# Optimization experiments

Hardware: AMD Instinct MI355X
Metric: run time of the kernel (lower is better)

Reference implementation:

```python
import jax, jax.numpy as jnp
import numpy as np

B, N, C = 4, 48 * 64, 256
H, W = 48, 64


def _positional_encodings(batch, dtype=jnp.float32):
    # (x^2, y^2, xy, x, y, 1) encoding; matches get_positional_encodings with intrinsics=None
    ys = jnp.linspace(-1.0, 1.0, H, dtype=dtype)
    xs = jnp.linspace(-1.0, 1.0, W, dtype=dtype)
    p3 = jnp.tile(ys, W)            # [N] : ys repeated W times (torch .repeat(B, w))
    p4 = jnp.repeat(xs, H)          # [N] : each x repeated H times (repeat_interleave)
    pos = jnp.stack([p3 * p3, p4 * p4, p3 * p4, p3, p4, jnp.ones_like(p3)], axis=-1)  # [N,6]
    return jnp.broadcast_to(pos, (batch, N, 6))


def setup_inputs() -> dict:
    key = jax.random.key(0)
    k1, k2, k3, k4 = jax.random.split(key, 4)
    x1 = jax.random.normal(k1, (B, N, C), dtype=jnp.float32)
    x2 = jax.random.normal(k2, (B, N, C), dtype=jnp.float32)
    corr = jax.random.normal(k3, (B, 1, H, W, H, W), dtype=jnp.float32)
    W_proj = jax.random.normal(k4, (C + 6, C), dtype=jnp.float32) * (1.0 / np.sqrt(C + 6))
    b_proj = jnp.zeros((C,), dtype=jnp.float32)
    return {"x1": x1, "x2": x2, "corr": corr, "W_proj": W_proj, "b_proj": b_proj}


def reference(x1, x2, corr, W_proj, b_proj):
    b, n, c = x1.shape
    a = corr.reshape(b, n, n)                      # squeeze(1) + double flatten
    # dual softmax (row-wise * column-wise)
    s_row = jax.nn.softmax(a, axis=-1)
    s_col = jax.nn.softmax(a, axis=-2)
    attn_f1 = s_row * s_col                        # [B,N,N]
    attn_f2 = jnp.swapaxes(attn_f1, -2, -1)        # softmax(a^T,-1)*softmax(a^T,-2) == attn_f1^T

    pos = _positional_encodings(b, dtype=x1.dtype)
    v1 = jnp.concatenate([x1, pos], axis=2)        # [B,N,C+6]
    v2 = jnp.concatenate([x2, pos], axis=2)

    # bilinear products v^T @ attn @ v  -> [B, C+6, C+6]
    fund1 = jnp.einsum('bnc,bnm,bmd->bcd', v1, attn_f1, v1)
    fund2 = jnp.einsum('bnc,bnm,bmd->bcd', v2, attn_f2, v2)

    fund1 = jnp.swapaxes(fund1, -2, -1)
    fund2 = jnp.swapaxes(fund2, -2, -1)

    out1 = fund1 @ W_proj + b_proj                 # proj_fundamental
    out2 = fund2 @ W_proj + b_proj
    return (out2, out1)                            # (fundamental_2, fundamental_1)
```

## Files before the change

kernel.cpp:

```cpp
#include <hip/hip_runtime.h>
#include <math.h>

#define NB 4
#define NN 3072
#define NC 256
#define CP 262
#define KG 384
#define XW 528
#define MD 272
#define K3S 4
#define HH 48
#define WW 64
#define LOG2E 1.4426950408889634f

typedef short short8 __attribute__((ext_vector_type(8)));
typedef short short4v __attribute__((ext_vector_type(4)));
typedef float f32x4 __attribute__((ext_vector_type(4)));
typedef unsigned int uint4v __attribute__((ext_vector_type(4)));

__device__ __forceinline__ float fexp2(float x) {
#if __has_builtin(__builtin_amdgcn_exp2f)
    return __builtin_amdgcn_exp2f(x);
#else
    return __exp2f(x);
#endif
}

__device__ __forceinline__ void bsplit(float v, short& h, short& l) {
    unsigned u = __float_as_uint(v);
    h = (short)(u >> 16);
    float r = v - __uint_as_float(u & 0xFFFF0000u);
    l = (short)(__float_as_uint(r) >> 16);
}

__device__ __forceinline__ void fma4(float4& c, float a, float4 b) {
    c.x = fmaf(a, b.x, c.x);
    c.y = fmaf(a, b.y, c.y);
    c.z = fmaf(a, b.z, c.z);
    c.w = fmaf(a, b.w, c.w);
}

__global__ __launch_bounds__(256) void k_stats(const float* __restrict__ corr,
                                               const float* __restrict__ x1,
                                               const float* __restrict__ x2,
                                               float* __restrict__ pSum,
                                               float* __restrict__ rlS,
                                               short* __restrict__ Xh, short* __restrict__ Xl) {
    int bid = blockIdx.x;
    int t = threadIdx.x;
    if (bid < 384) {
        int cx = bid % 12;
        int b = (bid / 12) & 3;
        int ch = bid / 48;
        int m = cx * 256 + t;
        const float* p = corr + (size_t)b * NN * NN + (size_t)ch * 384 * NN + m;
        float s0 = 0.f, s1 = 0.f, s2 = 0.f, s3 = 0.f;
        for (int r = 0; r < 384; r += 4) {
            s0 += __expf(p[(size_t)(r + 0) * NN]);
            s1 += __expf(p[(size_t)(r + 1) * NN]);
            s2 += __expf(p[(size_t)(r + 2) * NN]);
            s3 += __expf(p[(size_t)(r + 3) * NN]);
        }
        pSum[((size_t)ch * NB + b) * NN + m] = (s0 + s1) + (s2 + s3);
    } else if (bid < 3456) {
        int rid = bid - 384;
        int b = rid / 768;
        int r0 = (rid - b * 768) * 4;
        int w = t >> 6, l = t & 63;
        int n = r0 + w;
        const float4* p = (const float4*)(corr + ((size_t)b * NN + n) * NN);
        float s = 0.f;
#pragma unroll
        for (int i = 0; i < 12; i++) {
            float4 v = p[l + i * 64];
            s += __expf(v.x) + __expf(v.y) + __expf(v.z) + __expf(v.w);
        }
#pragma unroll
        for (int off = 1; off < 64; off <<= 1) s += __shfl_xor(s, off);
        if (l == 0) rlS[b * NN + n] = __log2f(s);
    } else {
        int id = (bid - 3456) * 256 + t;
        int col = id % XW;
        int rest = id / XW;
        int kg = rest % KG;
        int b = rest / KG;
        short* ph = Xh + (size_t)id * 8;
        short* pl = Xl + (size_t)id * 8;
        if (col < 512) {
            const float* src = (col < 256 ? x1 : x2) + ((size_t)b * NN + kg * 8) * NC + (col & 255);
#pragma unroll
            for (int j = 0; j < 8; j++) {
                short hs, ls;
                bsplit(src[(size_t)j * NC], hs, ls);
                ph[j] = hs; pl[j] = ls;
            }
        } else {
            int c = col - 512;
#pragma unroll
            for (int j = 0; j < 8; j++) {
                int k = kg * 8 + j;
                int ip4 = k / HH;
                int ip3 = k - ip4 * HH;
                float p3 = -1.f + 2.f * (float)ip3 / 47.f;
                float p4 = -1.f + 2.f * (float)ip4 / 63.f;
                float v = 0.f;
                if (c == 0) v = p3 * p3;
                else if (c == 1) v = p4 * p4;
                else if (c == 2) v = p3 * p4;
                else if (c == 3) v = p3;
                else if (c == 4) v = p4;
                else if (c == 5) v = 1.f;
                short hs, ls;
                bsplit(v, hs, ls);
                ph[j] = hs; pl[j] = ls;
            }
        }
    }
}

__global__ __launch_bounds__(256) void k_comb(const float* __restrict__ pSum,
                                              float* __restrict__ ccS) {
    int idx = blockIdx.x * 256 + threadIdx.x;
    float s = 0.f;
#pragma unroll
    for (int ch = 0; ch < 8; ch++) s += pSum[(size_t)ch * NB * NN + idx];
    ccS[idx] = __log2f(s);
}

struct SMemMain {
    unsigned AH[2][48 * 32];
    unsigned AL[2][48 * 32];
    float ccsh[NN];
};
union SMemU {
    SMemMain m;
    float pdump[2 * 64 * 12];
};

#define LOAD_B4(PH, PL, BHF, BLF)                                            \
    {                                                                        \
        _Pragma("unroll") for (int i_ = 0; i_ < 4; i_++) {                   \
            BHF[i_] = *(const short8*)((PH) + i_ * 128);                     \
            BLF[i_] = *(const short8*)((PL) + i_ * 128);                     \
        }                                                                    \
    }

#define READ_AFRAGS3(BUFH, BUFL, UNIT, AHF, ALF)                             \
    {                                                                        \
        _Pragma("unroll") for (int fr_ = 0; fr_ < 3; fr_++) {                \
            int rowr_ = fr_ * 16 + row16;                                    \
            int uidx_ = rowr_ * 32 + (((UNIT) ^ (rowr_ & 7)) << 2);          \
            AHF[fr_] = *(const short8*)&(BUFH)[uidx_];                       \
            ALF[fr_] = *(const short8*)&(BUFL)[uidx_];                       \
        }                                                                    \
    }

#define MFMA_CLUSTER34(AHF, ALF, BHF, BLF)                                                         \
    {                                                                                              \
        _Pragma("unroll") for (int fr_ = 0; fr_ < 3; fr_++)                                        \
        _Pragma("unroll") for (int i_ = 0; i_ < 4; i_++)                                           \
            acc[fr_][i_] = __builtin_amdgcn_mfma_f32_16x16x32_bf16(AHF[fr_], BHF[i_], acc[fr_][i_], 0, 0, 0); \
        _Pragma("unroll") for (int fr_ = 0; fr_ < 3; fr_++)                                        \
        _Pragma("unroll") for (int i_ = 0; i_ < 4; i_++)                                           \
            acc[fr_][i_] = __builtin_amdgcn_mfma_f32_16x16x32_bf16(AHF[fr_], BLF[i_], acc[fr_][i_], 0, 0, 0); \
        _Pragma("unroll") for (int fr_ = 0; fr_ < 3; fr_++)                                        \
        _Pragma("unroll") for (int i_ = 0; i_ < 4; i_++)                                           \
            acc[fr_][i_] = __builtin_amdgcn_mfma_f32_16x16x32_bf16(ALF[fr_], BHF[i_], acc[fr_][i_], 0, 0, 0); \
    }

#define POS_CLUSTER3(AHF, ALF, PBH, PBL)                                                           \
    {                                                                                              \
        _Pragma("unroll") for (int fr_ = 0; fr_ < 3; fr_++) {                                      \
            accP[fr_] = __builtin_amdgcn_mfma_f32_16x16x32_bf16(AHF[fr_], (PBH), accP[fr_], 0, 0, 0); \
            accP[fr_] = __builtin_amdgcn_mfma_f32_16x16x32_bf16(AHF[fr_], (PBL), accP[fr_], 0, 0, 0); \
            accP[fr_] = __builtin_amdgcn_mfma_f32_16x16x32_bf16(ALF[fr_], (PBH), accP[fr_], 0, 0, 0); \
        }                                                                                          \
    }

#define STAGE_A8(DSTH, DSTL, PC)                                                                  \
    {                                                                                             \
        f32x4 ccv0 = *(const f32x4*)&ccsh[(PC) * 64 + g * 8];                                     \
        f32x4 ccv1 = *(const f32x4*)&ccsh[(PC) * 64 + g * 8 + 4];                                 \
        float ev[8];                                                                              \
        _Pragma("unroll") for (int q_ = 0; q_ < 4; q_++) {                                        \
            ev[q_]     = fexp2(fmaf(C2, cr0[q_], rmn) - ccv0[q_]);                                \
            ev[4 + q_] = fexp2(fmaf(C2, cr1[q_], rmn) - ccv1[q_]);                                \
        }                                                                                         \
        uint4v hi, lo;                                                                            \
        _Pragma("unroll") for (int q_ = 0; q_ < 4; q_++) {                                        \
            unsigned u0 = __float_as_uint(ev[2 * q_]);                                            \
            unsigned u1 = __float_as_uint(ev[2 * q_ + 1]);                                        \
            hi[q_] = __builtin_amdgcn_perm(u1, u0, 0x07060302u);                                  \
            float r0_ = ev[2 * q_] - __uint_as_float(u0 & 0xffff0000u);                           \
            float r1_ = ev[2 * q_ + 1] - __uint_as_float(u1 & 0xffff0000u);                       \
            lo[q_] = __builtin_amdgcn_perm(__float_as_uint(r1_), __float_as_uint(r0_), 0x07060302u); \
        }                                                                                         \
        *(uint4v*)&(DSTH)[widx] = hi;                                                             \
        *(uint4v*)&(DSTL)[widx] = lo;                                                             \
    }

__global__ __launch_bounds__(512, 2) void k2_mfma(const float* __restrict__ corr,
        const short* __restrict__ Xh, const short* __restrict__ Xl,
        const float* __restrict__ rlS, const float* __restrict__ ccS,
        short* __restrict__ Zh, short* __restrict__ Zl) {
    __shared__ SMemU sm;
    float* ccsh = sm.m.ccsh;

    const float C2 = 2.f * LOG2E;
    const size_t BSTEP = (size_t)4 * XW * 8;

    int bid = blockIdx.x;
    int xcd = bid & 7, sub = bid >> 3;
    int b = xcd >> 1;
    int rowblk = (xcd & 1) + (sub << 1);
    int n0 = rowblk * 48;

    int t = threadIdx.x;
    int w = t >> 6, l = t & 63;
    int row16 = l & 15, slot = l >> 4;
    bool duty6 = (w == 6);
    bool duty7 = (w == 7);
    bool writer = (t < 384);
    int wrow = t >> 3, g = t & 7;
    int widx = wrow * 32 + ((g ^ (wrow & 7)) << 2);

    {
        const f32x4* src = (const f32x4*)(ccS + (size_t)b * NN);
        for (int i = t; i < NN / 4; i += 512) ((f32x4*)ccsh)[i] = src[i];
    }

    const float* corrR = corr;
    float rmn = 0.f;
    if (writer) {
        corrR = corr + ((size_t)b * NN + n0 + wrow) * NN + g * 8;
        rmn = -rlS[b * NN + n0 + wrow];
    }

    int col0 = w * 64 + row16;
    const short* bh = Xh + ((size_t)(b * KG + slot) * XW + col0) * 8;
    const short* bl = Xl + ((size_t)(b * KG + slot) * XW + col0) * 8;

    f32x4 acc[3][4];
    f32x4 accP[3];
    const f32x4 zz = {0.f, 0.f, 0.f, 0.f};
#pragma unroll
    for (int fr = 0; fr < 3; fr++) {
#pragma unroll
        for (int i = 0; i < 4; i++) acc[fr][i] = zz;
        accP[fr] = zz;
    }

    short8 BhA[4], BlA[4], BhB[4], BlB[4];
    short8 P0h = {0,0,0,0,0,0,0,0}, P0l = P0h, P1h = P0h, P1l = P0h;
    LOAD_B4(bh, bl, BhA, BlA);

    f32x4 cr0, cr1;
    __syncthreads();
    if (writer) {
        cr0 = *(const f32x4*)(corrR);
        cr1 = *(const f32x4*)(corrR + 4);
        STAGE_A8(sm.m.AH[0], sm.m.AL[0], 0);
        cr0 = *(const f32x4*)(corrR + 64);
        cr1 = *(const f32x4*)(corrR + 68);
    }
    asm volatile("s_waitcnt lgkmcnt(0)" ::: "memory");
    __builtin_amdgcn_s_barrier();

    int cur = 0;
    for (int p = 0; p < 48; ++p) {
        const unsigned* AHc = &sm.m.AH[cur][0];
        const unsigned* ALc = &sm.m.AL[cur][0];
        unsigned* AHn = &sm.m.AH[cur ^ 1][0];
        unsigned* ALn = &sm.m.AL[cur ^ 1][0];
        short8 Ah[3], Al[3];
        READ_AFRAGS3(AHc, ALc, slot, Ah, Al);
        bh += BSTEP; bl += BSTEP;
        LOAD_B4(bh, bl, BhB, BlB);
        if (duty6) {
            size_t o0 = ((size_t)(b * KG + p * 8 + slot) * XW + 512 + row16) * 8;
            P0h = *(const short8*)(Xh + o0);
            P0l = *(const short8*)(Xl + o0);
        }
        MFMA_CLUSTER34(Ah, Al, BhA, BlA);
        if (duty6) POS_CLUSTER3(Ah, Al, P0h, P0l);
        READ_AFRAGS3(AHc, ALc, 4 + slot, Ah, Al);
        if (p < 47) {
            bh += BSTEP; bl += BSTEP;
            LOAD_B4(bh, bl, BhA, BlA);
        }
        if (duty7) {
            size_t o1 = ((size_t)(b * KG + p * 8 + 4 + slot) * XW + 512 + row16) * 8;
            P1h = *(const short8*)(Xh + o1);
            P1l = *(const short8*)(Xl + o1);
        }
        if (writer) {
            int pc = (p + 1 < 48) ? p + 1 : 47;
            STAGE_A8(AHn, ALn, pc);
            int pn = (p + 2 < 48) ? p + 2 : 47;
            cr0 = *(const f32x4*)(corrR + pn * 64);
            cr1 = *(const f32x4*)(corrR + pn * 64 + 4);
        }
        MFMA_CLUSTER34(Ah, Al, BhB, BlB);
        if (duty7) POS_CLUSTER3(Ah, Al, P1h, P1l);
        asm volatile("s_waitcnt lgkmcnt(0)" ::: "memory");
        __builtin_amdgcn_s_barrier();
        cur ^= 1;
    }

#pragma unroll
    for (int fr = 0; fr < 3; fr++) {
        int kgz = rowblk * 6 + fr * 2 + (slot >> 1);
        int jb = (slot & 1) << 2;
#pragma unroll
        for (int i = 0; i < 4; i++) {
            int colv = w * 64 + i * 16 + row16;
            size_t off = ((size_t)(b * KG + kgz) * XW + colv) * 8 + jb;
            short4v zh, zl;
#pragma unroll
            for (int r = 0; r < 4; r++) {
                short hs, ls; bsplit(acc[fr][i][r], hs, ls);
                zh[r] = hs; zl[r] = ls;
            }
            *(short4v*)(Zh + off) = zh;
            *(short4v*)(Zl + off) = zl;
        }
    }
    if (w >= 6) {
#pragma unroll
        for (int fr = 0; fr < 3; fr++)
            *(f32x4*)&sm.pdump[(size_t)((w - 6) * 64 + l) * 12 + fr * 4] = accP[fr];
    }
    __syncthreads();
    if (t < 192) {
        int fr = t >> 6, ll = t & 63;
        int sl = ll >> 4, r16 = ll & 15;
        f32x4 s = *(const f32x4*)&sm.pdump[(size_t)ll * 12 + fr * 4]
                + *(const f32x4*)&sm.pdump[(size_t)(64 + ll) * 12 + fr * 4];
        int kgz = rowblk * 6 + fr * 2 + (sl >> 1);
        int jb = (sl & 1) << 2;
        size_t off = ((size_t)(b * KG + kgz) * XW + 512 + r16) * 8 + jb;
        short4v zh, zl;
#pragma unroll
        for (int r = 0; r < 4; r++) {
            short hs, ls; bsplit(s[r], hs, ls);
            zh[r] = hs; zl[r] = ls;
        }
        *(short4v*)(Zh + off) = zh;
        *(short4v*)(Zl + off) = zl;
    }
}

__global__ __launch_bounds__(256) void k3_mfma(const short* __restrict__ Xh, const short* __restrict__ Xl,
                                               const short* __restrict__ Zh, const short* __restrict__ Zl,
                                               float* __restrict__ Mpart) {
    int tile = blockIdx.x;
    int rt = tile / 3, ct = tile % 3;
    int mb = blockIdx.y;
    int mat = mb >> 2, b = mb & 3;
    int split = blockIdx.z;

    const int O0[4] = {0, 6, 12, 17};
    int r0f = O0[rt], rNf = O0[rt + 1] - r0f;
    int c0f = O0[ct], cNf = O0[ct + 1] - c0f;

    int t = threadIdx.x;
    int w = t >> 6, l = t & 63;
    int row16 = l & 15, slot = l >> 4;
    int wr = w >> 1, wc = w & 1;
    int rh = (rNf + 1) >> 1;
    int rbeg = r0f + (wr ? rh : 0);
    int rcnt = wr ? (rNf - rh) : rh;
    int chh = (cNf + 1) >> 1;
    int cbeg = c0f + (wc ? chh : 0);
    int ccnt = wc ? (cNf - chh) : chh;

    const short *Ah_, *Al_, *Bh_, *Bl_;
    int abase, bbase;
    if (mat == 0) { Ah_ = Xh; Al_ = Xl; Bh_ = Zh; Bl_ = Zl; abase = 0; bbase = 0; }
    else          { Ah_ = Zh; Al_ = Zl; Bh_ = Xh; Bl_ = Xl; abase = 256; bbase = 256; }

    int acol[3], bcol[3];
#pragma unroll
    for (int i = 0; i < 3; i++) {
        int fa = rbeg + i;
        acol[i] = ((fa < 16) ? (abase + fa * 16) : 512) + row16;
        int fb = cbeg + i;
        bcol[i] = ((fb < 16) ? (bbase + fb * 16) : 512) + row16;
    }

    f32x4 acc[3][3];
    const f32x4 zz = {0.f, 0.f, 0.f, 0.f};
#pragma unroll
    for (int i = 0; i < 3; i++)
#pragma unroll
        for (int j = 0; j < 3; j++) acc[i][j] = zz;

    for (int it = 0; it < 24; it++) {
        int kg = split * 96 + it * 4 + slot;
        size_t base = (size_t)(b * KG + kg) * XW;
        short8 Ah[3], Al[3], Bhf[3], Blf[3];
#pragma unroll
        for (int i = 0; i < 3; i++) {
            if (i < rcnt) {
                Ah[i] = *(const short8*)(Ah_ + (base + acol[i]) * 8);
                Al[i] = *(const short8*)(Al_ + (base + acol[i]) * 8);
            }
            if (i < ccnt) {
                Bhf[i] = *(const short8*)(Bh_ + (base + bcol[i]) * 8);
                Blf[i] = *(const short8*)(Bl_ + (base + bcol[i]) * 8);
            }
        }
#pragma unroll
        for (int i = 0; i < 3; i++) {
            if (i < rcnt) {
#pragma unroll
                for (int j = 0; j < 3; j++) {
                    if (j < ccnt) {
                        acc[i][j] = __builtin_amdgcn_mfma_f32_16x16x32_bf16(Ah[i], Bhf[j], acc[i][j], 0, 0, 0);
                        acc[i][j] = __builtin_amdgcn_mfma_f32_16x16x32_bf16(Al[i], Bhf[j], acc[i][j], 0, 0, 0);
                        acc[i][j] = __builtin_amdgcn_mfma_f32_16x16x32_bf16(Ah[i], Blf[j], acc[i][j], 0, 0, 0);
                    }
                }
            }
        }
    }

    float* Mp = Mpart + (size_t)(mb * K3S + split) * (MD * MD);
#pragma unroll
    for (int i = 0; i < 3; i++) {
        if (i < rcnt) {
#pragma unroll
            for (int j = 0; j < 3; j++) {
                if (j < ccnt) {
                    int r = (rbeg + i) * 16 + slot * 4;
                    int c = (cbeg + j) * 16 + row16;
#pragma unroll
                    for (int q = 0; q < 4; q++)
                        Mp[(size_t)(r + q) * MD + c] = acc[i][j][q];
                }
            }
        }
    }
}

__global__ __launch_bounds__(256) void k_mcombine(const float* __restrict__ Mpart, float* __restrict__ M) {
    const int per = MD * MD;
    int f4 = blockIdx.x * 256 + threadIdx.x;
    if (f4 >= (8 * per) / 4) return;
    int e = f4 * 4;
    int mb = e / per;
    int off = e - mb * per;
    const float* src = Mpart + (size_t)mb * K3S * per + off;
    float4 s = make_float4(0.f, 0.f, 0.f, 0.f);
#pragma unroll
    for (int sp = 0; sp < K3S; sp++) {
        float4 v = *(const float4*)(src + (size_t)sp * per);
        s.x += v.x; s.y += v.y; s.z += v.z; s.w += v.w;
    }
    *(float4*)(M + (size_t)mb * per + off) = s;
}

__global__ __launch_bounds__(256) void k4_proj(const float* __restrict__ M, const float* __restrict__ Wp,
                                               const float* __restrict__ bp, float* __restrict__ out) {
    int i0 = blockIdx.x * 16;
    int b = blockIdx.y;
    int mat = blockIdx.z;
    const float* Mp = M + (size_t)(mat * 4 + b) * (MD * MD);
    int t = threadIdx.x;
    int jt = t & 63, it = t >> 6;
    int j = jt * 4;
    float4 a0 = make_float4(0.f, 0.f, 0.f, 0.f), a1 = a0, a2 = a0, a3 = a0;
#pragma unroll 2
    for (int k = 0; k < CP; k++) {
        float4 w = *(const float4*)(Wp + (size_t)k * NC + j);
        float4 g = *(const float4*)(Mp + (size_t)k * MD + i0 + it * 4);
        fma4(a0, g.x, w); fma4(a1, g.y, w); fma4(a2, g.z, w); fma4(a3, g.w, w);
    }
    float4 bb = *(const float4*)(bp + j);
    a0.x += bb.x; a0.y += bb.y; a0.z += bb.z; a0.w += bb.w;
    a1.x += bb.x; a1.y += bb.y; a1.z += bb.z; a1.w += bb.w;
    a2.x += bb.x; a2.y += bb.y; a2.z += bb.z; a2.w += bb.w;
    a3.x += bb.x; a3.y += bb.y; a3.z += bb.z; a3.w += bb.w;
    float* ob = out + (mat == 0 ? (size_t)NB * CP * NC : (size_t)0) + (size_t)b * CP * NC;
    int i = i0 + it * 4;
    if (i + 0 < CP) *(float4*)(ob + (size_t)(i + 0) * NC + j) = a0;
    if (i + 1 < CP) *(float4*)(ob + (size_t)(i + 1) * NC + j) = a1;
    if (i + 2 < CP) *(float4*)(ob + (size_t)(i + 2) * NC + j) = a2;
    if (i + 3 < CP) *(float4*)(ob + (size_t)(i + 3) * NC + j) = a3;
}

extern "C" void kernel_launch(void* const* d_in, const int* in_sizes, int n_in,
                              void* d_out, int out_size, void* d_ws, size_t ws_size,
                              hipStream_t stream) {
    const float* x1 = (const float*)d_in[0];
    const float* x2 = (const float*)d_in[1];
    const float* corr = (const float*)d_in[2];
    const float* Wp = (const float*)d_in[3];
    const float* bp = (const float*)d_in[4];
    float* out = (float*)d_out;
    float* w = (float*)d_ws;

    const size_t XSZ = (size_t)NB * KG * XW * 8;

    size_t o = 0;
    float* rlS = w + o;   o += NB * NN;
    float* ccS = w + o;   o += NB * NN;
    float* pSum = w + o;  o += 8 * NB * NN;
    short* Xh = (short*)(w + o); o += XSZ / 2;
    short* Xl = (short*)(w + o); o += XSZ / 2;
    short* Zh = (short*)(w + o); o += XSZ / 2;
    short* Zl = (short*)(w + o); o += XSZ / 2;
    float* Mpart = w + o; o += (size_t)8 * K3S * MD * MD;
    float* M = w + o;     o += (size_t)8 * MD * MD;

    k_stats<<<dim3(6624), dim3(256), 0, stream>>>(corr, x1, x2, pSum, rlS, Xh, Xl);
    k_comb<<<dim3(48), dim3(256), 0, stream>>>(pSum, ccS);
    k2_mfma<<<dim3(256), dim3(512), 0, stream>>>(corr, Xh, Xl, rlS, ccS, Zh, Zl);
    k3_mfma<<<dim3(9, 8, K3S), dim3(256), 0, stream>>>(Xh, Xl, Zh, Zl, Mpart);
    k_mcombine<<<dim3(578), dim3(256), 0, stream>>>(Mpart, M);
    k4_proj<<<dim3(17, NB, 2), dim3(256), 0, stream>>>(M, Wp, bp, out);
}
```

Before: 256.4 us.

## Fuse softmax statistics and X split into main kernel with grid barriers

```diff
diff --git a/kernel.cpp b/kernel.cpp
--- a/kernel.cpp
+++ b/kernel.cpp
@@ -38,93 +38,6 @@
     c.y = fmaf(a, b.y, c.y);
     c.z = fmaf(a, b.z, c.z);
     c.w = fmaf(a, b.w, c.w);
-}
-
-__global__ __launch_bounds__(256) void k_stats(const float* __restrict__ corr,
-                                               const float* __restrict__ x1,
-                                               const float* __restrict__ x2,
-                                               float* __restrict__ pSum,
-                                               float* __restrict__ rlS,
-                                               short* __restrict__ Xh, short* __restrict__ Xl) {
-    int bid = blockIdx.x;
-    int t = threadIdx.x;
-    if (bid < 384) {
-        int cx = bid % 12;
-        int b = (bid / 12) & 3;
-        int ch = bid / 48;
-        int m = cx * 256 + t;
-        const float* p = corr + (size_t)b * NN * NN + (size_t)ch * 384 * NN + m;
-        float s0 = 0.f, s1 = 0.f, s2 = 0.f, s3 = 0.f;
-        for (int r = 0; r < 384; r += 4) {
-            s0 += __expf(p[(size_t)(r + 0) * NN]);
-            s1 += __expf(p[(size_t)(r + 1) * NN]);
-            s2 += __expf(p[(size_t)(r + 2) * NN]);
-            s3 += __expf(p[(size_t)(r + 3) * NN]);
-        }
-        pSum[((size_t)ch * NB + b) * NN + m] = (s0 + s1) + (s2 + s3);
-    } else if (bid < 3456) {
-        int rid = bid - 384;
-        int b = rid / 768;
-        int r0 = (rid - b * 768) * 4;
-        int w = t >> 6, l = t & 63;
-        int n = r0 + w;
-        const float4* p = (const float4*)(corr + ((size_t)b * NN + n) * NN);
-        float s = 0.f;
-#pragma unroll
-        for (int i = 0; i < 12; i++) {
-            float4 v = p[l + i * 64];
-            s += __expf(v.x) + __expf(v.y) + __expf(v.z) + __expf(v.w);
-        }
-#pragma unroll
-        for (int off = 1; off < 64; off <<= 1) s += __shfl_xor(s, off);
-        if (l == 0) rlS[b * NN + n] = __log2f(s);
-    } else {
-        int id = (bid - 3456) * 256 + t;
-        int col = id % XW;
-        int rest = id / XW;
-        int kg = rest % KG;
-        int b = rest / KG;
-        short* ph = Xh + (size_t)id * 8;
-        short* pl = Xl + (size_t)id * 8;
-        if (col < 512) {
-            const float* src = (col < 256 ? x1 : x2) + ((size_t)b * NN + kg * 8) * NC + (col & 255);
-#pragma unroll
-            for (int j = 0; j < 8; j++) {
-                short hs, ls;
-                bsplit(src[(size_t)j * NC], hs, ls);
-                ph[j] = hs; pl[j] = ls;
-            }
-        } else {
-            int c = col - 512;
-#pragma unroll
-            for (int j = 0; j < 8; j++) {
-                int k = kg * 8 + j;
-                int ip4 = k / HH;
-                int ip3 = k - ip4 * HH;
-                float p3 = -1.f + 2.f * (float)ip3 / 47.f;
-                float p4 = -1.f + 2.f * (float)ip4 / 63.f;
-                float v = 0.f;
-                if (c == 0) v = p3 * p3;
-                else if (c == 1) v = p4 * p4;
-                else if (c == 2) v = p3 * p4;
-                else if (c == 3) v = p3;
-                else if (c == 4) v = p4;
-                else if (c == 5) v = 1.f;
-                short hs, ls;
-                bsplit(v, hs, ls);
-                ph[j] = hs; pl[j] = ls;
-            }
-        }
-    }
-}
-
-__global__ __launch_bounds__(256) void k_comb(const float* __restrict__ pSum,
-                                              float* __restrict__ ccS) {
-    int idx = blockIdx.x * 256 + threadIdx.x;
-    float s = 0.f;
-#pragma unroll
-    for (int ch = 0; ch < 8; ch++) s += pSum[(size_t)ch * NB * NN + idx];
-    ccS[idx] = __log2f(s);
 }
 
 struct SMemMain {
@@ -199,11 +112,14 @@
         *(uint4v*)&(DSTL)[widx] = lo;                                                             \
     }
 
-__global__ __launch_bounds__(512, 2) void k2_mfma(const float* __restrict__ corr,
-        const short* __restrict__ Xh, const short* __restrict__ Xl,
-        const float* __restrict__ rlS, const float* __restrict__ ccS,
-        short* __restrict__ Zh, short* __restrict__ Zl) {
+__global__ __launch_bounds__(512, 2) void k2_fused(const float* __restrict__ corr,
+        const float* __restrict__ x1, const float* __restrict__ x2,
+        short* __restrict__ Xh, short* __restrict__ Xl,
+        short* __restrict__ Zh, short* __restrict__ Zl,
+        float* __restrict__ colpart, float* __restrict__ ccS,
+        int* __restrict__ ctr1, int* __restrict__ ctr2) {
     __shared__ SMemU sm;
+    __shared__ float rls_sh[48];
     float* ccsh = sm.m.ccsh;
 
     const float C2 = 2.f * LOG2E;
@@ -218,23 +134,122 @@
     int t = threadIdx.x;
     int w = t >> 6, l = t & 63;
     int row16 = l & 15, slot = l >> 4;
+    const f32x4 zz = {0.f, 0.f, 0.f, 0.f};
+
+    for (int i = t; i < NN; i += 512) ccsh[i] = 0.f;
+    __syncthreads();
+
+    f32x4 cpa[12];
+#pragma unroll
+    for (int i = 0; i < 12; i++) cpa[i] = zz;
+    for (int rr = 0; rr < 6; rr++) {
+        const f32x4* rp = (const f32x4*)(corr + ((size_t)b * NN + n0 + w * 6 + rr) * NN);
+        float rsum = 0.f;
+#pragma unroll
+        for (int i = 0; i < 12; i++) {
+            f32x4 v = rp[l + i * 64];
+            f32x4 e;
+            e[0] = __expf(v[0]); e[1] = __expf(v[1]);
+            e[2] = __expf(v[2]); e[3] = __expf(v[3]);
+            cpa[i] += e;
+            rsum += (e[0] + e[1]) + (e[2] + e[3]);
+        }
+#pragma unroll
+        for (int off = 1; off < 64; off <<= 1) rsum += __shfl_xor(rsum, off);
+        if (l == 0) rls_sh[w * 6 + rr] = __log2f(rsum);
+    }
+    for (int wv = 0; wv < 8; wv++) {
+        if (w == wv) {
+#pragma unroll
+            for (int i = 0; i < 12; i++) {
+                f32x4* dst = (f32x4*)&ccsh[4 * (l + 64 * i)];
+                *dst += cpa[i];
+            }
+        }
+        __syncthreads();
+    }
+
+    for (int it = t; it < 3168; it += 512) {
+        int col = it % 528;
+        int kgl = it / 528;
+        int kg = rowblk * 6 + kgl;
+        short* ph = Xh + ((size_t)(b * KG + kg) * XW + col) * 8;
+        short* pl = Xl + ((size_t)(b * KG + kg) * XW + col) * 8;
+        if (col < 512) {
+            const float* src = (col < 256 ? x1 : x2) + ((size_t)b * NN + kg * 8) * NC + (col & 255);
+#pragma unroll
+            for (int j = 0; j < 8; j++) {
+                short hs, ls;
+                bsplit(src[(size_t)j * NC], hs, ls);
+                ph[j] = hs; pl[j] = ls;
+            }
+        } else {
+            int c = col - 512;
+#pragma unroll
+            for (int j = 0; j < 8; j++) {
+                int k = kg * 8 + j;
+                int ip4 = k / HH;
+                int ip3 = k - ip4 * HH;
+                float p3 = -1.f + 2.f * (float)ip3 / 47.f;
+                float p4 = -1.f + 2.f * (float)ip4 / 63.f;
+                float v = 0.f;
+                if (c == 0) v = p3 * p3;
+                else if (c == 1) v = p4 * p4;
+                else if (c == 2) v = p3 * p4;
+                else if (c == 3) v = p3;
+                else if (c == 4) v = p4;
+                else if (c == 5) v = 1.f;
+                short hs, ls;
+                bsplit(v, hs, ls);
+                ph[j] = hs; pl[j] = ls;
+            }
+        }
+    }
+
+    {
+        float* cp = colpart + (size_t)(b * 64 + rowblk) * NN;
+        for (int i = t; i < NN; i += 512) cp[i] = ccsh[i];
+    }
+    __syncthreads();
+    if (t == 0) {
+        __threadfence();
+        atomicAdd(ctr1 + b, 1);
+        while (__hip_atomic_load(ctr1 + b, __ATOMIC_ACQUIRE, __HIP_MEMORY_SCOPE_AGENT) < 64)
+            __builtin_amdgcn_s_sleep(8);
+    }
+    __syncthreads();
+
+    if (t < 48) {
+        const float* cp = colpart + (size_t)(b * 64) * NN + rowblk * 48 + t;
+        float s0 = 0.f, s1 = 0.f, s2 = 0.f, s3 = 0.f;
+        for (int s = 0; s < 64; s += 4) {
+            s0 += cp[(size_t)(s + 0) * NN];
+            s1 += cp[(size_t)(s + 1) * NN];
+            s2 += cp[(size_t)(s + 2) * NN];
+            s3 += cp[(size_t)(s + 3) * NN];
+        }
+        ccS[(size_t)b * NN + rowblk * 48 + t] = __log2f((s0 + s1) + (s2 + s3));
+    }
+    __syncthreads();
+    if (t == 0) {
+        __threadfence();
+        atomicAdd(ctr2 + b, 1);
+        while (__hip_atomic_load(ctr2 + b, __ATOMIC_ACQUIRE, __HIP_MEMORY_SCOPE_AGENT) < 64)
+            __builtin_amdgcn_s_sleep(8);
+    }
+    __syncthreads();
+
+    for (int i = t; i < NN; i += 512) ccsh[i] = ccS[(size_t)b * NN + i];
+
     bool duty6 = (w == 6);
     bool duty7 = (w == 7);
     bool writer = (t < 384);
     int wrow = t >> 3, g = t & 7;
     int widx = wrow * 32 + ((g ^ (wrow & 7)) << 2);
 
-    {
-        const f32x4* src = (const f32x4*)(ccS + (size_t)b * NN);
-        for (int i = t; i < NN / 4; i += 512) ((f32x4*)ccsh)[i] = src[i];
-    }
-
     const float* corrR = corr;
     float rmn = 0.f;
-    if (writer) {
-        corrR = corr + ((size_t)b * NN + n0 + wrow) * NN + g * 8;
-        rmn = -rlS[b * NN + n0 + wrow];
-    }
+    if (writer) corrR = corr + ((size_t)b * NN + n0 + wrow) * NN + g * 8;
 
     int col0 = w * 64 + row16;
     const short* bh = Xh + ((size_t)(b * KG + slot) * XW + col0) * 8;
@@ -242,7 +257,6 @@
 
     f32x4 acc[3][4];
     f32x4 accP[3];
-    const f32x4 zz = {0.f, 0.f, 0.f, 0.f};
 #pragma unroll
     for (int fr = 0; fr < 3; fr++) {
 #pragma unroll
@@ -257,6 +271,7 @@
     f32x4 cr0, cr1;
     __syncthreads();
     if (writer) {
+        rmn = -rls_sh[wrow];
         cr0 = *(const f32x4*)(corrR);
         cr1 = *(const f32x4*)(corrR + 4);
         STAGE_A8(sm.m.AH[0], sm.m.AL[0], 0);
@@ -503,9 +518,9 @@
     const size_t XSZ = (size_t)NB * KG * XW * 8;
 
     size_t o = 0;
-    float* rlS = w + o;   o += NB * NN;
-    float* ccS = w + o;   o += NB * NN;
-    float* pSum = w + o;  o += 8 * NB * NN;
+    int* ctrs = (int*)(w + o); o += 8;
+    float* ccS = w + o;     o += NB * NN;
+    float* colpart = w + o; o += (size_t)NB * 64 * NN;
     short* Xh = (short*)(w + o); o += XSZ / 2;
     short* Xl = (short*)(w + o); o += XSZ / 2;
     short* Zh = (short*)(w + o); o += XSZ / 2;
@@ -513,9 +528,9 @@
     float* Mpart = w + o; o += (size_t)8 * K3S * MD * MD;
     float* M = w + o;     o += (size_t)8 * MD * MD;
 
-    k_stats<<<dim3(6624), dim3(256), 0, stream>>>(corr, x1, x2, pSum, rlS, Xh, Xl);
-    k_comb<<<dim3(48), dim3(256), 0, stream>>>(pSum, ccS);
-    k2_mfma<<<dim3(256), dim3(512), 0, stream>>>(corr, Xh, Xl, rlS, ccS, Zh, Zl);
+    hipMemsetAsync(ctrs, 0, 8 * sizeof(int), stream);
+    k2_fused<<<dim3(256), dim3(512), 0, stream>>>(corr, x1, x2, Xh, Xl, Zh, Zl,
+                                                  colpart, ccS, ctrs, ctrs + 4);
     k3_mfma<<<dim3(9, 8, K3S), dim3(256), 0, stream>>>(Xh, Xl, Zh, Zl, Mpart);
     k_mcombine<<<dim3(578), dim3(256), 0, stream>>>(Mpart, M);
     k4_proj<<<dim3(17, NB, 2), dim3(256), 0, stream>>>(M, Wp, bp, out);
```

After: 292.2 us. 14.0% more time.

## Fuse row and column softmax statistics into a single pass over corr

Applied to the files above, without the earlier changes.

```diff
diff --git a/kernel.cpp b/kernel.cpp
--- a/kernel.cpp
+++ b/kernel.cpp
@@ -43,43 +43,53 @@
 __global__ __launch_bounds__(256) void k_stats(const float* __restrict__ corr,
                                                const float* __restrict__ x1,
                                                const float* __restrict__ x2,
-                                               float* __restrict__ pSum,
+                                               float* __restrict__ colpart,
                                                float* __restrict__ rlS,
                                                short* __restrict__ Xh, short* __restrict__ Xl) {
     int bid = blockIdx.x;
     int t = threadIdx.x;
-    if (bid < 384) {
-        int cx = bid % 12;
-        int b = (bid / 12) & 3;
-        int ch = bid / 48;
-        int m = cx * 256 + t;
-        const float* p = corr + (size_t)b * NN * NN + (size_t)ch * 384 * NN + m;
-        float s0 = 0.f, s1 = 0.f, s2 = 0.f, s3 = 0.f;
-        for (int r = 0; r < 384; r += 4) {
-            s0 += __expf(p[(size_t)(r + 0) * NN]);
-            s1 += __expf(p[(size_t)(r + 1) * NN]);
-            s2 += __expf(p[(size_t)(r + 2) * NN]);
-            s3 += __expf(p[(size_t)(r + 3) * NN]);
-        }
-        pSum[((size_t)ch * NB + b) * NN + m] = (s0 + s1) + (s2 + s3);
-    } else if (bid < 3456) {
-        int rid = bid - 384;
-        int b = rid / 768;
-        int r0 = (rid - b * 768) * 4;
+    if (bid < 1024) {
+        int chunk = bid & 255;
+        int b = bid >> 8;
+        int r0 = chunk * 12;
+        const float* base = corr + ((size_t)b * NN + r0) * NN;
+        f32x4 colacc[3];
+        const f32x4 zz = {0.f, 0.f, 0.f, 0.f};
+#pragma unroll
+        for (int c = 0; c < 3; c++) colacc[c] = zz;
+        float rowpart[12];
+#pragma unroll 2
+        for (int r = 0; r < 12; r++) {
+            float rp = 0.f;
+#pragma unroll
+            for (int cp = 0; cp < 3; cp++) {
+                f32x4 v = *(const f32x4*)(base + (size_t)r * NN + cp * 1024 + t * 4);
+                f32x4 e;
+                e[0] = __expf(v[0]); e[1] = __expf(v[1]);
+                e[2] = __expf(v[2]); e[3] = __expf(v[3]);
+                colacc[cp] += e;
+                rp += (e[0] + e[1]) + (e[2] + e[3]);
+            }
+            rowpart[r] = rp;
+        }
+        __shared__ float red[4][12];
         int w = t >> 6, l = t & 63;
-        int n = r0 + w;
-        const float4* p = (const float4*)(corr + ((size_t)b * NN + n) * NN);
-        float s = 0.f;
-#pragma unroll
-        for (int i = 0; i < 12; i++) {
-            float4 v = p[l + i * 64];
-            s += __expf(v.x) + __expf(v.y) + __expf(v.z) + __expf(v.w);
-        }
-#pragma unroll
-        for (int off = 1; off < 64; off <<= 1) s += __shfl_xor(s, off);
-        if (l == 0) rlS[b * NN + n] = __log2f(s);
+#pragma unroll
+        for (int r = 0; r < 12; r++) {
+            float rp = rowpart[r];
+#pragma unroll
+            for (int off = 1; off < 64; off <<= 1) rp += __shfl_xor(rp, off);
+            if (l == 0) red[w][r] = rp;
+        }
+        __syncthreads();
+        if (t < 12)
+            rlS[b * NN + r0 + t] = __log2f(red[0][t] + red[1][t] + red[2][t] + red[3][t]);
+        float* cp = colpart + (size_t)(b * 256 + chunk) * NN;
+#pragma unroll
+        for (int c = 0; c < 3; c++)
+            *(f32x4*)(cp + c * 1024 + t * 4) = colacc[c];
     } else {
-        int id = (bid - 3456) * 256 + t;
+        int id = (bid - 1024) * 256 + t;
         int col = id % XW;
         int rest = id / XW;
         int kg = rest % KG;
@@ -118,13 +128,20 @@
     }
 }
 
-__global__ __launch_bounds__(256) void k_comb(const float* __restrict__ pSum,
+__global__ __launch_bounds__(256) void k_comb(const float* __restrict__ colpart,
                                               float* __restrict__ ccS) {
     int idx = blockIdx.x * 256 + threadIdx.x;
-    float s = 0.f;
-#pragma unroll
-    for (int ch = 0; ch < 8; ch++) s += pSum[(size_t)ch * NB * NN + idx];
-    ccS[idx] = __log2f(s);
+    int b = idx / NN;
+    int m = idx - b * NN;
+    const float* cp = colpart + (size_t)b * 256 * NN + m;
+    float s0 = 0.f, s1 = 0.f, s2 = 0.f, s3 = 0.f;
+    for (int ch = 0; ch < 256; ch += 4) {
+        s0 += cp[(size_t)(ch + 0) * NN];
+        s1 += cp[(size_t)(ch + 1) * NN];
+        s2 += cp[(size_t)(ch + 2) * NN];
+        s3 += cp[(size_t)(ch + 3) * NN];
+    }
+    ccS[idx] = __log2f((s0 + s1) + (s2 + s3));
 }
 
 struct SMemMain {
@@ -281,8 +298,10 @@
             P0h = *(const short8*)(Xh + o0);
             P0l = *(const short8*)(Xl + o0);
         }
+        __builtin_amdgcn_s_setprio(1);
         MFMA_CLUSTER34(Ah, Al, BhA, BlA);
         if (duty6) POS_CLUSTER3(Ah, Al, P0h, P0l);
+        __builtin_amdgcn_s_setprio(0);
         READ_AFRAGS3(AHc, ALc, 4 + slot, Ah, Al);
         if (p < 47) {
             bh += BSTEP; bl += BSTEP;
@@ -300,8 +319,10 @@
             cr0 = *(const f32x4*)(corrR + pn * 64);
             cr1 = *(const f32x4*)(corrR + pn * 64 + 4);
         }
+        __builtin_amdgcn_s_setprio(1);
         MFMA_CLUSTER34(Ah, Al, BhB, BlB);
         if (duty7) POS_CLUSTER3(Ah, Al, P1h, P1l);
+        __builtin_amdgcn_s_setprio(0);
         asm volatile("s_waitcnt lgkmcnt(0)" ::: "memory");
         __builtin_amdgcn_s_barrier();
         cur ^= 1;
@@ -503,9 +524,9 @@
     const size_t XSZ = (size_t)NB * KG * XW * 8;
 
     size_t o = 0;
-    float* rlS = w + o;   o += NB * NN;
-    float* ccS = w + o;   o += NB * NN;
-    float* pSum = w + o;  o += 8 * NB * NN;
+    float* rlS = w + o;     o += NB * NN;
+    float* ccS = w + o;     o += NB * NN;
+    float* colpart = w + o; o += (size_t)NB * 256 * NN;
     short* Xh = (short*)(w + o); o += XSZ / 2;
     short* Xl = (short*)(w + o); o += XSZ / 2;
     short* Zh = (short*)(w + o); o += XSZ / 2;
@@ -513,8 +534,8 @@
     float* Mpart = w + o; o += (size_t)8 * K3S * MD * MD;
     float* M = w + o;     o += (size_t)8 * MD * MD;
 
-    k_stats<<<dim3(6624), dim3(256), 0, stream>>>(corr, x1, x2, pSum, rlS, Xh, Xl);
-    k_comb<<<dim3(48), dim3(256), 0, stream>>>(pSum, ccS);
+    k_stats<<<dim3(4192), dim3(256), 0, stream>>>(corr, x1, x2, colpart, rlS, Xh, Xl);
+    k_comb<<<dim3(48), dim3(256), 0, stream>>>(colpart, ccS);
     k2_mfma<<<dim3(256), dim3(512), 0, stream>>>(corr, Xh, Xl, rlS, ccS, Zh, Zl);
     k3_mfma<<<dim3(9, 8, K3S), dim3(256), 0, stream>>>(Xh, Xl, Zh, Zl, Mpart);
     k_mcombine<<<dim3(578), dim3(256), 0, stream>>>(Mpart, M);
```

Result: no change. 257.8 us (+0.6%).
